# Performance work log

Hardware: AMD Instinct MI355X
Metric: run time of the kernel (lower is better)

The kernel has to match this reference:

```python
import jax, jax.numpy as jnp
import numpy as np

B, N, K = 8192, 2048, 4  # batch, nodes, neighbors (original: 45, 168, 4)


def _collect_and_transfer(x, adj):
    # x: (B, N), adj: (N, K) int indices of neighbors.
    # Original builds, per node i, a (B, K) block of gathered neighbor values,
    # stacks to (N, B, K), then raw-reshapes (view) to (B, 1, K, N).
    g = jnp.transpose(x[:, adj], (1, 0, 2))   # (N, B, K)
    return g.reshape(x.shape[0], 1, K, adj.shape[0])  # memory reinterpretation, as in .view


def reference(x, label, adj, conv_w, conv_b, lin_w, lin_b):
    a = jnp.concatenate([_collect_and_transfer(x, adj),
                         _collect_and_transfer(label, adj)], axis=1)  # (B, 2, K, N)
    # Conv2d(2 -> 1, kernel=(1,4), stride=(1,4)): (B, 1, K, N//4)
    y = jax.lax.conv_general_dilated(
        a, conv_w, window_strides=(1, 4), padding='VALID',
        dimension_numbers=('NCHW', 'OIHW', 'NCHW'))
    y = jax.nn.relu(y + conv_b[None, :, None, None])
    y = y.reshape(B, N)              # K * (N//4) == N
    return y @ lin_w.T + lin_b       # Linear(N, N)


def setup_inputs() -> dict:
    key = jax.random.key(0)
    k1, k2, k3, k4, k5 = jax.random.split(key, 5)
    return {
        'x': jax.random.normal(k1, (B, N), dtype=jnp.float32),
        'label': jax.random.normal(k2, (B, N), dtype=jnp.float32),
        'adj': jax.random.randint(k3, (N, K), 0, N, dtype=jnp.int32),
        'conv_w': jax.random.normal(k4, (1, 2, 1, 4), dtype=jnp.float32) * 0.1,
        'conv_b': jnp.zeros((1,), dtype=jnp.float32),
        'lin_w': jax.random.normal(k5, (N, N), dtype=jnp.float32) * 0.02,
        'lin_b': jnp.zeros((N,), dtype=jnp.float32),
    }
```

## Files before the change

### kernel.cpp

```cpp
#include <hip/hip_runtime.h>

typedef __bf16 bf16;
typedef bf16 bf16x8 __attribute__((ext_vector_type(8)));
typedef float f32x4 __attribute__((ext_vector_type(4)));
typedef unsigned short ushort;
typedef ushort ushort4v __attribute__((ext_vector_type(4)));

#define BB 8192
#define NN 2048

__device__ __forceinline__ void async16(const void* g, void* l) {
    __builtin_amdgcn_global_load_lds(
        (__attribute__((address_space(1))) void*)(void*)g,
        (__attribute__((address_space(3))) void*)l,
        16, 0, 0);
}

__global__ __launch_bounds__(256) void conv_gather(
    const float* __restrict__ x, const float* __restrict__ label,
    const int* __restrict__ adj, const float* __restrict__ cw,
    const float* __restrict__ cb, bf16* __restrict__ V) {
    __shared__ float4 sxl[NN];
    const int bb0 = blockIdx.x * 2;
    const int t   = threadIdx.x;

    const float4* x0 = (const float4*)(x     + (size_t)bb0 * NN);
    const float4* x1 = (const float4*)(x     + (size_t)(bb0 + 1) * NN);
    const float4* l0 = (const float4*)(label + (size_t)bb0 * NN);
    const float4* l1 = (const float4*)(label + (size_t)(bb0 + 1) * NN);
#pragma unroll
    for (int q = 0; q < 2; ++q) {
        int i = q * 256 + t;
        float4 a = x0[i], b = l0[i], c = x1[i], d = l1[i];
        int n0i = i * 4;
        int sx  = (i >> 1) & 7;
        sxl[(n0i + 0) ^ sx] = make_float4(a.x, b.x, c.x, d.x);
        sxl[(n0i + 1) ^ sx] = make_float4(a.y, b.y, c.y, d.y);
        sxl[(n0i + 2) ^ sx] = make_float4(a.z, b.z, c.z, d.z);
        sxl[(n0i + 3) ^ sx] = make_float4(a.w, b.w, c.w, d.w);
    }
    const float w0 = cw[0], w1 = cw[1], w2 = cw[2], w3 = cw[3];
    const float w4 = cw[4], w5 = cw[5], w6 = cw[6], w7 = cw[7];
    const float bias = cb[0];

    const int4* adj4 = (const int4*)adj;
    int4 a[8];
#pragma unroll
    for (int j = 0; j < 8; ++j) a[j] = adj4[t * 8 + j];

    __syncthreads();

    bf16 o0[8], o1[8];
#pragma unroll
    for (int j = 0; j < 8; ++j) {
        int4 aa = a[j];
        float4 p0 = sxl[aa.x ^ ((aa.x >> 3) & 7)];
        float4 p1 = sxl[aa.y ^ ((aa.y >> 3) & 7)];
        float4 p2 = sxl[aa.z ^ ((aa.z >> 3) & 7)];
        float4 p3 = sxl[aa.w ^ ((aa.w >> 3) & 7)];
        float v0 = bias
                 + w0 * p0.x + w1 * p1.x + w2 * p2.x + w3 * p3.x
                 + w4 * p0.y + w5 * p1.y + w6 * p2.y + w7 * p3.y;
        float v1 = bias
                 + w0 * p0.z + w1 * p1.z + w2 * p2.z + w3 * p3.z
                 + w4 * p0.w + w5 * p1.w + w6 * p2.w + w7 * p3.w;
        o0[j] = (bf16)fmaxf(v0, 0.0f);
        o1[j] = (bf16)fmaxf(v1, 0.0f);
    }
    *(bf16x8*)(V + (size_t)bb0 * NN + t * 8)       = *(const bf16x8*)o0;
    *(bf16x8*)(V + (size_t)(bb0 + 1) * NN + t * 8) = *(const bf16x8*)o1;
}

__global__ __launch_bounds__(256) void transp_cvtw(
    const ushort* __restrict__ V, ushort* __restrict__ Y,
    const float* __restrict__ W, bf16* __restrict__ Wb) {
    const int b = blockIdx.x;
    if (b >= 4096) {
        size_t i = (size_t)(b - 4096) * 256 + threadIdx.x;
        float4 v0 = ((const float4*)W)[i * 2 + 0];
        float4 v1 = ((const float4*)W)[i * 2 + 1];
        bf16x8 o;
        o[0] = (bf16)v0.x; o[1] = (bf16)v0.y; o[2] = (bf16)v0.z; o[3] = (bf16)v0.w;
        o[4] = (bf16)v1.x; o[5] = (bf16)v1.y; o[6] = (bf16)v1.z; o[7] = (bf16)v1.w;
        ((bf16x8*)Wb)[i] = o;
        return;
    }
    __shared__ __attribute__((aligned(16))) ushort tile[64][68];
    const int g0 = (b & 31) * 64;
    const int p0 = (b >> 5) * 64;
    const int c  = threadIdx.x & 15;
    const int r4 = threadIdx.x >> 4;

#pragma unroll
    for (int pass = 0; pass < 4; ++pass) {
        int r = pass * 16 + r4;
        ushort4v v = *(const ushort4v*)(V + (size_t)(p0 + r) * NN + g0 + c * 4);
        *(ushort4v*)&tile[r][c * 4] = v;
    }
    __syncthreads();
    ushort4v rv[4];
#pragma unroll
    for (int j = 0; j < 4; ++j)
        rv[j] = *(const ushort4v*)&tile[c * 4 + j][r4 * 4];
#pragma unroll
    for (int q = 0; q < 4; ++q) {
        ushort4v o;
        o.x = rv[0][q]; o.y = rv[1][q]; o.z = rv[2][q]; o.w = rv[3][q];
        *(ushort4v*)(Y + (size_t)(g0 + r4 * 4 + q) * BB + p0 + c * 4) = o;
    }
}

__global__ __launch_bounds__(512, 2) void gemm_bt(
    const bf16* __restrict__ A, const bf16* __restrict__ W,
    const float* __restrict__ bias, float* __restrict__ out) {
    __shared__ __attribute__((aligned(16))) bf16 sA[2][16384];
    __shared__ __attribute__((aligned(16))) bf16 sB[2][16384];

    const int t    = threadIdx.x;
    const int lane = t & 63;
    const int wv   = t >> 6;
    const int wm   = wv & 1;
    const int wn   = wv >> 1;
    const int l16  = lane & 15;
    const int l4   = lane >> 4;

    const int xcd = blockIdx.x & 7;
    const int loc = blockIdx.x >> 3;
    const int bx  = xcd * 4 + (loc >> 3);
    const int by  = loc & 7;
    const int m0  = bx * 256;
    const int n0  = by * 256;

    const int r8  = t >> 3;
    const int c8  = ((t & 7) ^ (r8 & 7)) * 8;
    const int dst = t * 8;

    const int sw    = l16 & 7;
    const int aOff0 = (wm * 128 + l16) * 64 + ((l4    ) ^ sw) * 8;
    const int aOff1 = (wm * 128 + l16) * 64 + ((l4 + 4) ^ sw) * 8;
    const int bOff0 = (wn * 64  + l16) * 64 + ((l4    ) ^ sw) * 8;
    const int bOff1 = (wn * 64  + l16) * 64 + ((l4 + 4) ^ sw) * 8;

    f32x4  acc[8][4] = {};
    bf16x8 aR[4][2], bR[4][2];

#define GBAR()  asm volatile("s_barrier" ::: "memory")
#define LGKM0() do { asm volatile("s_waitcnt lgkmcnt(0)" ::: "memory"); \
                     __builtin_amdgcn_sched_barrier(0); } while (0)
#define VMW6()  asm volatile("s_waitcnt vmcnt(6)" ::: "memory")
#define VMW0()  asm volatile("s_waitcnt vmcnt(0)" ::: "memory")

#define STG(G, rb, kt, lp) do {                                           \
        const bf16* _s = (G) + (size_t)((rb) + r8) * 2048 + (kt) + c8;    \
        async16(_s, (lp) + dst);                                          \
        async16(_s + (size_t)64 * 2048, (lp) + 4096 + dst);               \
    } while (0)

#define LDA(sp, mh) do {                                                  \
        const bf16* _p = (sp) + (mh) * 4096;                              \
        aR[0][0] = *(const bf16x8*)(_p + aOff0);                          \
        aR[0][1] = *(const bf16x8*)(_p + aOff1);                          \
        aR[1][0] = *(const bf16x8*)(_p + 1024 + aOff0);                   \
        aR[1][1] = *(const bf16x8*)(_p + 1024 + aOff1);                   \
        aR[2][0] = *(const bf16x8*)(_p + 2048 + aOff0);                   \
        aR[2][1] = *(const bf16x8*)(_p + 2048 + aOff1);                   \
        aR[3][0] = *(const bf16x8*)(_p + 3072 + aOff0);                   \
        aR[3][1] = *(const bf16x8*)(_p + 3072 + aOff1);                   \
    } while (0)

#define LDB(sp, nh) do {                                                  \
        const bf16* _p = (sp) + (nh) * 2048;                              \
        bR[(nh)*2+0][0] = *(const bf16x8*)(_p + bOff0);                   \
        bR[(nh)*2+0][1] = *(const bf16x8*)(_p + bOff1);                   \
        bR[(nh)*2+1][0] = *(const bf16x8*)(_p + 1024 + bOff0);            \
        bR[(nh)*2+1][1] = *(const bf16x8*)(_p + 1024 + bOff1);            \
    } while (0)

#define MM(mh, nh) do {                                                   \
        __builtin_amdgcn_s_setprio(1);                                    \
        _Pragma("unroll")                                                 \
        for (int _ks = 0; _ks < 2; ++_ks)                                 \
            _Pragma("unroll")                                             \
            for (int _mf = 0; _mf < 4; ++_mf)                             \
                _Pragma("unroll")                                         \
                for (int _nf = 0; _nf < 2; ++_nf)                         \
                    acc[(mh)*4+_mf][(nh)*2+_nf] =                         \
                        __builtin_amdgcn_mfma_f32_16x16x32_bf16(          \
                            aR[_mf][_ks], bR[(nh)*2+_nf][_ks],            \
                            acc[(mh)*4+_mf][(nh)*2+_nf], 0, 0, 0);        \
        __builtin_amdgcn_s_setprio(0);                                    \
    } while (0)

    bf16* const sA0 = &sA[0][0]; bf16* const sA1 = &sA[1][0];
    bf16* const sB0 = &sB[0][0]; bf16* const sB1 = &sB[1][0];

    STG(A, m0,       0,  sA0);
    STG(A, m0 + 128, 0,  sA0 + 8192);
    STG(W, n0,       0,  sB0);
    STG(W, n0 + 128, 0,  sB0 + 8192);
    STG(W, n0,       64, sB1);
    STG(W, n0 + 128, 64, sB1 + 8192);
    STG(A, m0,       64, sA1);
    VMW6();
    GBAR();

    for (int i = 0; i < 15; ++i) {
        const int kb = i * 128;
        LDA(sA0, 0); LDB(sB0, 0);
        STG(A, m0 + 128, kb + 64, sA1 + 8192);
        GBAR(); LGKM0();
        MM(0, 0);
        GBAR();
        LDB(sB0, 1);
        GBAR(); LGKM0();
        MM(0, 1);
        GBAR();
        LDA(sA0, 1);
        STG(W, n0, kb + 128, sB0);
        GBAR(); LGKM0();
        MM(1, 0);
        GBAR();
        STG(W, n0 + 128, kb + 128, sB0 + 8192);
        STG(A, m0,       kb + 128, sA0);
        GBAR(); LGKM0();
        MM(1, 1);
        VMW6();
        GBAR();
        LDA(sA1, 0); LDB(sB1, 0);
        STG(A, m0 + 128, kb + 128, sA0 + 8192);
        GBAR(); LGKM0();
        MM(0, 0);
        GBAR();
        LDB(sB1, 1);
        GBAR(); LGKM0();
        MM(0, 1);
        GBAR();
        LDA(sA1, 1);
        STG(W, n0, kb + 192, sB1);
        GBAR(); LGKM0();
        MM(1, 0);
        GBAR();
        STG(W, n0 + 128, kb + 192, sB1 + 8192);
        STG(A, m0,       kb + 192, sA1);
        GBAR(); LGKM0();
        MM(1, 1);
        VMW6();
        GBAR();
    }

    LDA(sA0, 0); LDB(sB0, 0);
    STG(A, m0 + 128, 1984, sA1 + 8192);
    GBAR(); LGKM0(); MM(0, 0); GBAR();
    LDB(sB0, 1);
    GBAR(); LGKM0(); MM(0, 1); GBAR();
    LDA(sA0, 1);
    GBAR(); LGKM0(); MM(1, 0); GBAR();
    GBAR(); LGKM0(); MM(1, 1);
    VMW0();
    GBAR();
    LDA(sA1, 0); LDB(sB1, 0);
    GBAR(); LGKM0(); MM(0, 0); GBAR();
    LDB(sB1, 1);
    GBAR(); LGKM0(); MM(0, 1); GBAR();
    LDA(sA1, 1);
    GBAR(); LGKM0(); MM(1, 0); GBAR();
    GBAR(); LGKM0(); MM(1, 1);

#pragma unroll
    for (int nf = 0; nf < 4; ++nf) {
        const int col = n0 + wn * 64 + nf * 16 + l16;
        const float bc = bias[col];
#pragma unroll
        for (int mf = 0; mf < 8; ++mf) {
            const size_t row = (size_t)(m0 + wm * 128 + mf * 16 + l4 * 4);
#pragma unroll
            for (int rr = 0; rr < 4; ++rr)
                out[(row + rr) * 2048 + col] = acc[mf][nf][rr] + bc;
        }
    }
#undef STG
#undef LDA
#undef LDB
#undef MM
#undef GBAR
#undef LGKM0
#undef VMW6
#undef VMW0
}

extern "C" void kernel_launch(void* const* d_in, const int* in_sizes, int n_in,
                              void* d_out, int out_size, void* d_ws, size_t ws_size,
                              hipStream_t stream) {
    (void)in_sizes; (void)n_in; (void)out_size; (void)ws_size;
    const float* x     = (const float*)d_in[0];
    const float* label = (const float*)d_in[1];
    const int*   adj   = (const int*)d_in[2];
    const float* cw    = (const float*)d_in[3];
    const float* cb    = (const float*)d_in[4];
    const float* lw    = (const float*)d_in[5];
    const float* lb    = (const float*)d_in[6];
    float* out = (float*)d_out;

    bf16* V  = (bf16*)d_out;
    bf16* Y2 = (bf16*)d_ws;
    bf16* Wb = (bf16*)((char*)d_ws + (size_t)2048 * 8192 * 2);

    conv_gather<<<BB / 2, 256, 0, stream>>>(x, label, adj, cw, cb, V);
    transp_cvtw<<<6144, 256, 0, stream>>>((const ushort*)V, (ushort*)Y2,
                                          lw, Wb);
    gemm_bt<<<dim3(256), 512, 0, stream>>>(Y2, Wb, lb, out);
}
```

Baseline: 269.3 us.

## Fuse transpose into conv-gather via packed layout read directly by GEMM loader

The conv/gather kernel now handles 8 batch rows per block, stages x/label in shared memory as bf16, and writes its output in a blocked layout that the GEMM's A-tile loader indexes directly. This removes the separate transpose kernel and its full round-trip of the intermediate through global memory. The weight fp32-to-bf16 conversion moves into extra blocks of the conv kernel. The risks are bf16 rounding of the inputs before the convolution, which is slightly less precise, and a more scattered address pattern for the GEMM A loads.

```diff
diff --git a/kernel.cpp b/kernel.cpp
--- a/kernel.cpp
+++ b/kernel.cpp
@@ -16,29 +16,32 @@
         16, 0, 0);
 }
 
-__global__ __launch_bounds__(256) void conv_gather(
+__global__ __launch_bounds__(256) void conv_gather_t(
     const float* __restrict__ x, const float* __restrict__ label,
     const int* __restrict__ adj, const float* __restrict__ cw,
-    const float* __restrict__ cb, bf16* __restrict__ V) {
-    __shared__ float4 sxl[NN];
-    const int bb0 = blockIdx.x * 2;
+    const float* __restrict__ cb, bf16* __restrict__ Vp,
+    const float* __restrict__ W, bf16* __restrict__ Wb) {
+    const int blk = blockIdx.x;
     const int t   = threadIdx.x;
 
-    const float4* x0 = (const float4*)(x     + (size_t)bb0 * NN);
-    const float4* x1 = (const float4*)(x     + (size_t)(bb0 + 1) * NN);
-    const float4* l0 = (const float4*)(label + (size_t)bb0 * NN);
-    const float4* l1 = (const float4*)(label + (size_t)(bb0 + 1) * NN);
-#pragma unroll
-    for (int q = 0; q < 2; ++q) {
-        int i = q * 256 + t;
-        float4 a = x0[i], b = l0[i], c = x1[i], d = l1[i];
-        int n0i = i * 4;
-        int sx  = (i >> 1) & 7;
-        sxl[(n0i + 0) ^ sx] = make_float4(a.x, b.x, c.x, d.x);
-        sxl[(n0i + 1) ^ sx] = make_float4(a.y, b.y, c.y, d.y);
-        sxl[(n0i + 2) ^ sx] = make_float4(a.z, b.z, c.z, d.z);
-        sxl[(n0i + 3) ^ sx] = make_float4(a.w, b.w, c.w, d.w);
-    }
+    if (blk >= 1024) {
+        const size_t f4 = ((size_t)(blk - 1024) * 256 + t) * 4;
+        const float4* Wf = (const float4*)W;
+        float4 v0 = Wf[f4 + 0], v1 = Wf[f4 + 1];
+        float4 v2 = Wf[f4 + 2], v3 = Wf[f4 + 3];
+        bf16x8 o0, o1;
+        o0[0]=(bf16)v0.x; o0[1]=(bf16)v0.y; o0[2]=(bf16)v0.z; o0[3]=(bf16)v0.w;
+        o0[4]=(bf16)v1.x; o0[5]=(bf16)v1.y; o0[6]=(bf16)v1.z; o0[7]=(bf16)v1.w;
+        o1[0]=(bf16)v2.x; o1[1]=(bf16)v2.y; o1[2]=(bf16)v2.z; o1[3]=(bf16)v2.w;
+        o1[4]=(bf16)v3.x; o1[5]=(bf16)v3.y; o1[6]=(bf16)v3.z; o1[7]=(bf16)v3.w;
+        ((bf16x8*)Wb)[(f4 >> 1) + 0] = o0;
+        ((bf16x8*)Wb)[(f4 >> 1) + 1] = o1;
+        return;
+    }
+
+    __shared__ bf16x8 sxl[NN];
+    const int bb0 = blk * 8;
+
     const float w0 = cw[0], w1 = cw[1], w2 = cw[2], w3 = cw[3];
     const float w4 = cw[4], w5 = cw[5], w6 = cw[6], w7 = cw[7];
     const float bias = cb[0];
@@ -48,65 +51,77 @@
 #pragma unroll
     for (int j = 0; j < 8; ++j) a[j] = adj4[t * 8 + j];
 
-    __syncthreads();
-
-    bf16 o0[8], o1[8];
+    bf16 oA[8][4], oB[8][4];
+
+#pragma unroll
+    for (int pp = 0; pp < 2; ++pp) {
+        if (pp) __syncthreads();
+        const int rb = bb0 + pp * 4;
+        const float4* x0 = (const float4*)(x     + (size_t)(rb + 0) * NN);
+        const float4* x1 = (const float4*)(x     + (size_t)(rb + 1) * NN);
+        const float4* x2 = (const float4*)(x     + (size_t)(rb + 2) * NN);
+        const float4* x3 = (const float4*)(x     + (size_t)(rb + 3) * NN);
+        const float4* l0 = (const float4*)(label + (size_t)(rb + 0) * NN);
+        const float4* l1 = (const float4*)(label + (size_t)(rb + 1) * NN);
+        const float4* l2 = (const float4*)(label + (size_t)(rb + 2) * NN);
+        const float4* l3 = (const float4*)(label + (size_t)(rb + 3) * NN);
+#pragma unroll
+        for (int q = 0; q < 2; ++q) {
+            int i = q * 256 + t;
+            float4 xa = x0[i], xb = x1[i], xc = x2[i], xd = x3[i];
+            float4 la = l0[i], lb = l1[i], lc = l2[i], ld = l3[i];
+            int n0i = i * 4;
+            int sx  = (i >> 1) & 7;
+            bf16x8 e;
+            e[0]=(bf16)xa.x; e[1]=(bf16)la.x; e[2]=(bf16)xb.x; e[3]=(bf16)lb.x;
+            e[4]=(bf16)xc.x; e[5]=(bf16)lc.x; e[6]=(bf16)xd.x; e[7]=(bf16)ld.x;
+            sxl[(n0i + 0) ^ sx] = e;
+            e[0]=(bf16)xa.y; e[1]=(bf16)la.y; e[2]=(bf16)xb.y; e[3]=(bf16)lb.y;
+            e[4]=(bf16)xc.y; e[5]=(bf16)lc.y; e[6]=(bf16)xd.y; e[7]=(bf16)ld.y;
+            sxl[(n0i + 1) ^ sx] = e;
+            e[0]=(bf16)xa.z; e[1]=(bf16)la.z; e[2]=(bf16)xb.z; e[3]=(bf16)lb.z;
+            e[4]=(bf16)xc.z; e[5]=(bf16)lc.z; e[6]=(bf16)xd.z; e[7]=(bf16)ld.z;
+            sxl[(n0i + 2) ^ sx] = e;
+            e[0]=(bf16)xa.w; e[1]=(bf16)la.w; e[2]=(bf16)xb.w; e[3]=(bf16)lb.w;
+            e[4]=(bf16)xc.w; e[5]=(bf16)lc.w; e[6]=(bf16)xd.w; e[7]=(bf16)ld.w;
+            sxl[(n0i + 3) ^ sx] = e;
+        }
+        __syncthreads();
+
+        bf16 (*od)[4] = pp ? oB : oA;
+#pragma unroll
+        for (int j = 0; j < 8; ++j) {
+            int4 aa = a[j];
+            bf16x8 p0 = sxl[aa.x ^ ((aa.x >> 3) & 7)];
+            bf16x8 p1 = sxl[aa.y ^ ((aa.y >> 3) & 7)];
+            bf16x8 p2 = sxl[aa.z ^ ((aa.z >> 3) & 7)];
+            bf16x8 p3 = sxl[aa.w ^ ((aa.w >> 3) & 7)];
+            float v0 = bias
+                + w0*(float)p0[0] + w1*(float)p1[0] + w2*(float)p2[0] + w3*(float)p3[0]
+                + w4*(float)p0[1] + w5*(float)p1[1] + w6*(float)p2[1] + w7*(float)p3[1];
+            float v1 = bias
+                + w0*(float)p0[2] + w1*(float)p1[2] + w2*(float)p2[2] + w3*(float)p3[2]
+                + w4*(float)p0[3] + w5*(float)p1[3] + w6*(float)p2[3] + w7*(float)p3[3];
+            float v2 = bias
+                + w0*(float)p0[4] + w1*(float)p1[4] + w2*(float)p2[4] + w3*(float)p3[4]
+                + w4*(float)p0[5] + w5*(float)p1[5] + w6*(float)p2[5] + w7*(float)p3[5];
+            float v3 = bias
+                + w0*(float)p0[6] + w1*(float)p1[6] + w2*(float)p2[6] + w3*(float)p3[6]
+                + w4*(float)p0[7] + w5*(float)p1[7] + w6*(float)p2[7] + w7*(float)p3[7];
+            od[j][0] = (bf16)fmaxf(v0, 0.0f);
+            od[j][1] = (bf16)fmaxf(v1, 0.0f);
+            od[j][2] = (bf16)fmaxf(v2, 0.0f);
+            od[j][3] = (bf16)fmaxf(v3, 0.0f);
+        }
+    }
+
+    bf16* vout = Vp + (size_t)blk * 16384 + t * 64;
 #pragma unroll
     for (int j = 0; j < 8; ++j) {
-        int4 aa = a[j];
-        float4 p0 = sxl[aa.x ^ ((aa.x >> 3) & 7)];
-        float4 p1 = sxl[aa.y ^ ((aa.y >> 3) & 7)];
-        float4 p2 = sxl[aa.z ^ ((aa.z >> 3) & 7)];
-        float4 p3 = sxl[aa.w ^ ((aa.w >> 3) & 7)];
-        float v0 = bias
-                 + w0 * p0.x + w1 * p1.x + w2 * p2.x + w3 * p3.x
-                 + w4 * p0.y + w5 * p1.y + w6 * p2.y + w7 * p3.y;
-        float v1 = bias
-                 + w0 * p0.z + w1 * p1.z + w2 * p2.z + w3 * p3.z
-                 + w4 * p0.w + w5 * p1.w + w6 * p2.w + w7 * p3.w;
-        o0[j] = (bf16)fmaxf(v0, 0.0f);
-        o1[j] = (bf16)fmaxf(v1, 0.0f);
-    }
-    *(bf16x8*)(V + (size_t)bb0 * NN + t * 8)       = *(const bf16x8*)o0;
-    *(bf16x8*)(V + (size_t)(bb0 + 1) * NN + t * 8) = *(const bf16x8*)o1;
-}
-
-__global__ __launch_bounds__(256) void transp_cvtw(
-    const ushort* __restrict__ V, ushort* __restrict__ Y,
-    const float* __restrict__ W, bf16* __restrict__ Wb) {
-    const int b = blockIdx.x;
-    if (b >= 4096) {
-        size_t i = (size_t)(b - 4096) * 256 + threadIdx.x;
-        float4 v0 = ((const float4*)W)[i * 2 + 0];
-        float4 v1 = ((const float4*)W)[i * 2 + 1];
-        bf16x8 o;
-        o[0] = (bf16)v0.x; o[1] = (bf16)v0.y; o[2] = (bf16)v0.z; o[3] = (bf16)v0.w;
-        o[4] = (bf16)v1.x; o[5] = (bf16)v1.y; o[6] = (bf16)v1.z; o[7] = (bf16)v1.w;
-        ((bf16x8*)Wb)[i] = o;
-        return;
-    }
-    __shared__ __attribute__((aligned(16))) ushort tile[64][68];
-    const int g0 = (b & 31) * 64;
-    const int p0 = (b >> 5) * 64;
-    const int c  = threadIdx.x & 15;
-    const int r4 = threadIdx.x >> 4;
-
-#pragma unroll
-    for (int pass = 0; pass < 4; ++pass) {
-        int r = pass * 16 + r4;
-        ushort4v v = *(const ushort4v*)(V + (size_t)(p0 + r) * NN + g0 + c * 4);
-        *(ushort4v*)&tile[r][c * 4] = v;
-    }
-    __syncthreads();
-    ushort4v rv[4];
-#pragma unroll
-    for (int j = 0; j < 4; ++j)
-        rv[j] = *(const ushort4v*)&tile[c * 4 + j][r4 * 4];
-#pragma unroll
-    for (int q = 0; q < 4; ++q) {
-        ushort4v o;
-        o.x = rv[0][q]; o.y = rv[1][q]; o.z = rv[2][q]; o.w = rv[3][q];
-        *(ushort4v*)(Y + (size_t)(g0 + r4 * 4 + q) * BB + p0 + c * 4) = o;
+        bf16x8 e;
+        e[0] = oA[j][0]; e[1] = oA[j][1]; e[2] = oA[j][2]; e[3] = oA[j][3];
+        e[4] = oB[j][0]; e[5] = oB[j][1]; e[6] = oB[j][2]; e[7] = oB[j][3];
+        *(bf16x8*)(vout + j * 8) = e;
     }
 }
 
@@ -150,10 +165,19 @@
 #define VMW6()  asm volatile("s_waitcnt vmcnt(6)" ::: "memory")
 #define VMW0()  asm volatile("s_waitcnt vmcnt(0)" ::: "memory")
 
-#define STG(G, rb, kt, lp) do {                                           \
-        const bf16* _s = (G) + (size_t)((rb) + r8) * 2048 + (kt) + c8;    \
+#define STGW(rb, kt, lp) do {                                             \
+        const bf16* _s = W + (size_t)((rb) + r8) * 2048 + (kt) + c8;      \
         async16(_s, (lp) + dst);                                          \
         async16(_s + (size_t)64 * 2048, (lp) + 4096 + dst);               \
+    } while (0)
+
+#define STGA(rb, kt, lp) do {                                             \
+        const int _m1 = (rb) + r8;                                        \
+        const int _kk = (kt) + c8;                                        \
+        const bf16* _s = A + ((size_t)(((_m1 & 3) << 8) + (_kk >> 3)) << 14) \
+                           + ((_m1 >> 2) << 3);                           \
+        async16(_s, (lp) + dst);                                          \
+        async16(_s + 128, (lp) + 4096 + dst);                             \
     } while (0)
 
 #define LDA(sp, mh) do {                                                  \
@@ -194,20 +218,20 @@
     bf16* const sA0 = &sA[0][0]; bf16* const sA1 = &sA[1][0];
     bf16* const sB0 = &sB[0][0]; bf16* const sB1 = &sB[1][0];
 
-    STG(A, m0,       0,  sA0);
-    STG(A, m0 + 128, 0,  sA0 + 8192);
-    STG(W, n0,       0,  sB0);
-    STG(W, n0 + 128, 0,  sB0 + 8192);
-    STG(W, n0,       64, sB1);
-    STG(W, n0 + 128, 64, sB1 + 8192);
-    STG(A, m0,       64, sA1);
+    STGA(m0,       0,  sA0);
+    STGA(m0 + 128, 0,  sA0 + 8192);
+    STGW(n0,       0,  sB0);
+    STGW(n0 + 128, 0,  sB0 + 8192);
+    STGW(n0,       64, sB1);
+    STGW(n0 + 128, 64, sB1 + 8192);
+    STGA(m0,       64, sA1);
     VMW6();
     GBAR();
 
     for (int i = 0; i < 15; ++i) {
         const int kb = i * 128;
         LDA(sA0, 0); LDB(sB0, 0);
-        STG(A, m0 + 128, kb + 64, sA1 + 8192);
+        STGA(m0 + 128, kb + 64, sA1 + 8192);
         GBAR(); LGKM0();
         MM(0, 0);
         GBAR();
@@ -216,18 +240,18 @@
         MM(0, 1);
         GBAR();
         LDA(sA0, 1);
-        STG(W, n0, kb + 128, sB0);
+        STGW(n0, kb + 128, sB0);
         GBAR(); LGKM0();
         MM(1, 0);
         GBAR();
-        STG(W, n0 + 128, kb + 128, sB0 + 8192);
-        STG(A, m0,       kb + 128, sA0);
+        STGW(n0 + 128, kb + 128, sB0 + 8192);
+        STGA(m0,       kb + 128, sA0);
         GBAR(); LGKM0();
         MM(1, 1);
         VMW6();
         GBAR();
         LDA(sA1, 0); LDB(sB1, 0);
-        STG(A, m0 + 128, kb + 128, sA0 + 8192);
+        STGA(m0 + 128, kb + 128, sA0 + 8192);
         GBAR(); LGKM0();
         MM(0, 0);
         GBAR();
@@ -236,12 +260,12 @@
         MM(0, 1);
         GBAR();
         LDA(sA1, 1);
-        STG(W, n0, kb + 192, sB1);
+        STGW(n0, kb + 192, sB1);
         GBAR(); LGKM0();
         MM(1, 0);
         GBAR();
-        STG(W, n0 + 128, kb + 192, sB1 + 8192);
-        STG(A, m0,       kb + 192, sA1);
+        STGW(n0 + 128, kb + 192, sB1 + 8192);
+        STGA(m0,       kb + 192, sA1);
         GBAR(); LGKM0();
         MM(1, 1);
         VMW6();
@@ -249,7 +273,7 @@
     }
 
     LDA(sA0, 0); LDB(sB0, 0);
-    STG(A, m0 + 128, 1984, sA1 + 8192);
+    STGA(m0 + 128, 1984, sA1 + 8192);
     GBAR(); LGKM0(); MM(0, 0); GBAR();
     LDB(sB0, 1);
     GBAR(); LGKM0(); MM(0, 1); GBAR();
@@ -278,7 +302,8 @@
                 out[(row + rr) * 2048 + col] = acc[mf][nf][rr] + bc;
         }
     }
-#undef STG
+#undef STGW
+#undef STGA
 #undef LDA
 #undef LDB
 #undef MM
@@ -301,12 +326,9 @@
     const float* lb    = (const float*)d_in[6];
     float* out = (float*)d_out;
 
-    bf16* V  = (bf16*)d_out;
-    bf16* Y2 = (bf16*)d_ws;
+    bf16* Vp = (bf16*)d_ws;
     bf16* Wb = (bf16*)((char*)d_ws + (size_t)2048 * 8192 * 2);
 
-    conv_gather<<<BB / 2, 256, 0, stream>>>(x, label, adj, cw, cb, V);
-    transp_cvtw<<<6144, 256, 0, stream>>>((const ushort*)V, (ushort*)Y2,
-                                          lw, Wb);
-    gemm_bt<<<dim3(256), 512, 0, stream>>>(Y2, Wb, lb, out);
+    conv_gather_t<<<2048, 256, 0, stream>>>(x, label, adj, cw, cb, Vp, lw, Wb);
+    gemm_bt<<<dim3(256), 512, 0, stream>>>(Vp, Wb, lb, out);
 }
```

Measured after the change: 267.2 us. No clear change (-0.8%).
